# Kernel tuning notes

Hardware: AMD Instinct MI355X
Metric: run time of the kernel (lower is better)

Reference implementation:

```python
import jax, jax.numpy as jnp
import numpy as np

NUM_HEADS = 16


def setup_inputs() -> dict:
    key = jax.random.key(0)
    k1, k2, k3, k4 = jax.random.split(key, 4)
    in_dim, out_dim = 1024, 1024
    x = jax.random.normal(k1, (4, 2048, in_dim), dtype=jnp.float32)
    # nn.Linear weights stored as [out, in]; we keep that convention.
    s = 1.0 / np.sqrt(in_dim)
    Wq = jax.random.uniform(k2, (out_dim, in_dim), jnp.float32, -s, s)
    Wk = jax.random.uniform(k3, (out_dim, in_dim), jnp.float32, -s, s)
    Wv = jax.random.uniform(k4, (out_dim, in_dim), jnp.float32, -s, s)
    return {"x": x, "Wq": Wq, "Wk": Wk, "Wv": Wv}


def reference(x, Wq, Wk, Wv):
    b, n, _ = x.shape
    out_dim = Wq.shape[0]
    h = NUM_HEADS
    d = out_dim // h  # head_dim

    def split_heads(t):  # [b,n,out] -> [b,h,n,d]
        return t.reshape(b, n, h, d).transpose(0, 2, 1, 3)

    q = split_heads(x @ Wq.T)
    k = split_heads(x @ Wk.T)
    v = split_heads(x @ Wv.T)

    scores = jnp.einsum("bhqd,bhkd->bhqk", q, k) / jnp.sqrt(jnp.float32(d))
    causal = jnp.tril(jnp.ones((n, n), dtype=bool))
    scores = jnp.where(causal, scores, -jnp.inf)
    attn = jax.nn.softmax(scores, axis=-1)
    out = jnp.einsum("bhqk,bhkd->bhqd", attn, v)
    return out.transpose(0, 2, 1, 3).reshape(b, n, out_dim)
```

## Files before the change

### kernel.cpp

```cpp
#include <hip/hip_runtime.h>

typedef __attribute__((ext_vector_type(8))) short short8;
typedef __attribute__((ext_vector_type(4))) short short4v;
typedef __attribute__((ext_vector_type(4))) float floatx4;
typedef __attribute__((ext_vector_type(16))) float floatx16;

#define GLOBAL_AS __attribute__((address_space(1)))
#define LDS_AS __attribute__((address_space(3)))

__device__ __forceinline__ short f2bs(float f) {
    union { float f; unsigned u; } v; v.f = f;
    unsigned r = v.u + 0x7fffu + ((v.u >> 16) & 1u);
    return (short)(r >> 16);
}

#if __has_builtin(__builtin_amdgcn_cvt_pk_bf16_f32)
typedef __attribute__((ext_vector_type(2))) __bf16 bf16x2;
__device__ __forceinline__ unsigned pk2(float a, float b) {
    union { bf16x2 v; unsigned u; } u;
    u.v = __builtin_amdgcn_cvt_pk_bf16_f32(a, b);
    return u.u;
}
#else
__device__ __forceinline__ unsigned pk2(float a, float b) {
    union { float f; unsigned u; } x, y; x.f = a; y.f = b;
    return ((y.u + 0x8000u) & 0xffff0000u) | ((x.u + 0x8000u) >> 16);
}
#endif

__global__ __launch_bounds__(256) void cast_all(const float* __restrict__ x,
                                                const float* __restrict__ Wq,
                                                const float* __restrict__ Wk,
                                                const float* __restrict__ Wv,
                                                short* __restrict__ xb,
                                                short* __restrict__ wb) {
    int b = blockIdx.x;
    int t = threadIdx.x;
    const float* src;
    short* dst;
    int idx;
    if (b < 8192) {
        src = x; dst = xb; idx = b * 1024 + t * 4;
    } else {
        int r = b - 8192;
        int wz = r >> 10;
        src = (wz == 0) ? Wq : (wz == 1) ? Wk : Wv;
        dst = wb + wz * (1 << 20);
        idx = (r & 1023) * 1024 + t * 4;
    }
    float4 v = *(const float4*)(src + idx);
    short4v o;
    o.x = f2bs(v.x); o.y = f2bs(v.y); o.z = f2bs(v.z); o.w = f2bs(v.w);
    *(short4v*)(dst + idx) = o;
}

__global__ __launch_bounds__(256) void qkv_gemm(const short* __restrict__ xb,
                                                const short* __restrict__ wb,
                                                short* __restrict__ qout,
                                                short* __restrict__ kout,
                                                short* __restrict__ vtout) {
    __shared__ short As[128 * 64];
    __shared__ short Bs[128 * 64];
    const int K = 1024;
    int tid = threadIdx.x;
    int lane = tid & 63;
    int wid = tid >> 6;
    int quad = lane >> 4;
    int l16 = lane & 15;
    int wm = (wid >> 1) * 64;
    int wn = (wid & 1) * 64;
    int bm = blockIdx.x * 128;
    int bn = blockIdx.y * 128;
    const short* W = wb + (size_t)blockIdx.z * K * 1024;

    floatx4 acc[4][4];
#pragma unroll
    for (int i = 0; i < 4; i++)
#pragma unroll
        for (int j = 0; j < 4; j++) acc[i][j] = (floatx4){0.f, 0.f, 0.f, 0.f};

    int srow = tid >> 3;
    int ssw = ((tid & 7) ^ (srow & 7)) * 8;

    for (int kk = 0; kk < K; kk += 64) {
        __syncthreads();
#pragma unroll
        for (int l = 0; l < 4; l++) {
            const short* g = xb + (size_t)(bm + srow + l * 32) * K + kk + ssw;
            __builtin_amdgcn_global_load_lds((const GLOBAL_AS void*)g,
                                             (LDS_AS void*)(As + tid * 8 + l * 2048), 16, 0, 0);
        }
#pragma unroll
        for (int l = 0; l < 4; l++) {
            const short* g = W + (size_t)(bn + srow + l * 32) * K + kk + ssw;
            __builtin_amdgcn_global_load_lds((const GLOBAL_AS void*)g,
                                             (LDS_AS void*)(Bs + tid * 8 + l * 2048), 16, 0, 0);
        }
        __syncthreads();

#pragma unroll
        for (int s = 0; s < 2; s++) {
            int slot = ((s * 4 + quad) ^ (l16 & 7)) * 8;
            short8 af[4], bf[4];
#pragma unroll
            for (int i = 0; i < 4; i++)
                af[i] = *(const short8*)(As + (wm + i * 16 + l16) * 64 + slot);
#pragma unroll
            for (int j = 0; j < 4; j++)
                bf[j] = *(const short8*)(Bs + (wn + j * 16 + l16) * 64 + slot);
#pragma unroll
            for (int i = 0; i < 4; i++)
#pragma unroll
                for (int j = 0; j < 4; j++)
                    acc[i][j] = __builtin_amdgcn_mfma_f32_16x16x32_bf16(af[i], bf[j], acc[i][j], 0, 0, 0);
        }
    }

    if (blockIdx.z == 2) {
#pragma unroll
        for (int i = 0; i < 4; i++) {
#pragma unroll
            for (int j = 0; j < 4; j++) {
                int m = bm + wm + i * 16 + quad * 4;
                int c = bn + wn + j * 16 + l16;
                int b = m >> 11, nn = m & 2047, h = c >> 6, dd = c & 63;
                short4v pk;
                pk.x = f2bs(acc[i][j][0]);
                pk.y = f2bs(acc[i][j][1]);
                pk.z = f2bs(acc[i][j][2]);
                pk.w = f2bs(acc[i][j][3]);
                *(short4v*)(vtout + ((size_t)(b * 16 + h) * 64 + dd) * 2048 + nn) = pk;
            }
        }
    } else {
        short* dst = (blockIdx.z == 0) ? qout : kout;
        float qs = (blockIdx.z == 0) ? 0.180336881f : 1.0f;
#pragma unroll
        for (int i = 0; i < 4; i++) {
#pragma unroll
            for (int j = 0; j < 4; j++) {
#pragma unroll
                for (int r = 0; r < 4; r++) {
                    int m = bm + wm + i * 16 + quad * 4 + r;
                    int c = bn + wn + j * 16 + l16;
                    dst[((size_t)((m >> 11) * 16 + (c >> 6)) * 2048 + (m & 2047)) * 64 + (c & 63)] =
                        f2bs(acc[i][j][r] * qs);
                }
            }
        }
    }
}

__global__ __launch_bounds__(256, 2) void attn(const short* __restrict__ q,
                                               const short* __restrict__ k,
                                               const short* __restrict__ vt,
                                               float* __restrict__ out) {
    __shared__ short Ks[128 * 64];
    __shared__ short Vs[64 * 128];
    __shared__ short Ps[4 * 32 * 136];

    int tid = threadIdx.x;
    int lane = tid & 63;
    int wid = tid >> 6;
    int l32 = lane & 31;
    int half = lane >> 5;

    int flat = blockIdx.x;
    int xcd = flat & 7;
    int slot = flat >> 3;
    int bh = xcd * 8 + (slot >> 3);
    int qx = slot & 7;
    int b = bh >> 4, h = bh & 15;

    const short* qp = q + (size_t)(b * 16 + h) * 2048 * 64;
    const short* kp = k + (size_t)(b * 16 + h) * 2048 * 64;
    const short* vp = vt + (size_t)(b * 16 + h) * 64 * 2048;

    int krow = tid >> 3;
    int ksw = ((tid & 7) ^ (krow & 7)) * 8;
    int vd = tid >> 4;
    int vc = tid & 15;
    int vsw = ((vc & 8) | ((vc ^ vd) & 7)) * 8;

    short* pw = Ps + wid * (32 * 136);

    for (int phase = 0; phase < 2; phase++) {
        int qt = (phase == 0) ? qx : (15 - qx);
        int qbase = qt * 128;
        int qrow_w = qbase + wid * 32;
        int qlane = qrow_w + l32;

        short8 qf[4];
#pragma unroll
        for (int s = 0; s < 4; s++)
            qf[s] = *(const short8*)(qp + (size_t)qlane * 64 + s * 16 + half * 8);

        floatx16 oacc[2];
#pragma unroll
        for (int nt = 0; nt < 2; nt++)
#pragma unroll
            for (int e = 0; e < 16; e++) oacc[nt][e] = 0.f;
        float rs = 0.f;

        int ntiles = qt + 1;
        for (int t = 0; t < ntiles; t++) {
            int kvb = t * 128;
            __syncthreads();
#pragma unroll
            for (int l = 0; l < 4; l++) {
                const short* g = kp + (size_t)(kvb + krow + l * 32) * 64 + ksw;
                __builtin_amdgcn_global_load_lds((const GLOBAL_AS void*)g,
                                                 (LDS_AS void*)(Ks + tid * 8 + l * 2048), 16, 0, 0);
            }
#pragma unroll
            for (int l = 0; l < 4; l++) {
                const short* g = vp + (size_t)(vd + l * 16) * 2048 + kvb + vsw;
                __builtin_amdgcn_global_load_lds((const GLOBAL_AS void*)g,
                                                 (LDS_AS void*)(Vs + tid * 8 + l * 2048), 16, 0, 0);
            }
            __syncthreads();

            floatx16 sacc[4];
#pragma unroll
            for (int kb = 0; kb < 4; kb++)
#pragma unroll
                for (int e = 0; e < 16; e++) sacc[kb][e] = 0.f;
#pragma unroll
            for (int s = 0; s < 4; s++) {
#pragma unroll
                for (int kb = 0; kb < 4; kb++) {
                    int key = kb * 32 + l32;
                    int c = s * 2 + half;
                    short8 kf = *(const short8*)(Ks + key * 64 + ((c ^ (key & 7)) * 8));
                    sacc[kb] = __builtin_amdgcn_mfma_f32_32x32x16_bf16(kf, qf[s], sacc[kb], 0, 0, 0);
                }
            }

            bool diag = (t == ntiles - 1) && (phase >= 0) && (kvb + 127 > qrow_w);
#pragma unroll
            for (int kb = 0; kb < 4; kb++) {
#pragma unroll
                for (int e = 0; e < 16; e++) {
                    float p = __builtin_amdgcn_exp2f(sacc[kb][e]);
                    if (diag) {
                        int key = kvb + kb * 32 + (e & 3) + 8 * (e >> 2) + 4 * half;
                        p = (key > qlane) ? 0.f : p;
                    }
                    sacc[kb][e] = p;
                    rs += p;
                }
#pragma unroll
                for (int g = 0; g < 4; g++) {
                    int2 wv;
                    wv.x = pk2(sacc[kb][4 * g], sacc[kb][4 * g + 1]);
                    wv.y = pk2(sacc[kb][4 * g + 2], sacc[kb][4 * g + 3]);
                    *(int2*)(pw + l32 * 136 + kb * 32 + g * 8 + 4 * half) = wv;
                }
            }
            __threadfence_block();

#pragma unroll
            for (int s = 0; s < 8; s++) {
                short8 pf = *(const short8*)(pw + l32 * 136 + s * 16 + half * 8);
#pragma unroll
                for (int nt = 0; nt < 2; nt++) {
                    int d = nt * 32 + l32;
                    int c = s * 2 + half;
                    int sl = (c & 8) | ((c ^ (d & 7)) & 7);
                    short8 vf = *(const short8*)(Vs + d * 128 + sl * 8);
                    oacc[nt] = __builtin_amdgcn_mfma_f32_32x32x16_bf16(pf, vf, oacc[nt], 0, 0, 0);
                }
            }
        }

        float tot = rs + __shfl_xor(rs, 32);
        float inv = 1.0f / tot;
        float invr[16];
#pragma unroll
        for (int e = 0; e < 16; e++)
            invr[e] = __shfl(inv, (e & 3) + 8 * (e >> 2) + 4 * half);
#pragma unroll
        for (int nt = 0; nt < 2; nt++) {
#pragma unroll
            for (int e = 0; e < 16; e++) {
                int r = (e & 3) + 8 * (e >> 2) + 4 * half;
                int nn = qrow_w + r;
                out[((size_t)b * 2048 + nn) * 1024 + h * 64 + nt * 32 + l32] = oacc[nt][e] * invr[e];
            }
        }
    }
}

extern "C" void kernel_launch(void* const* d_in, const int* in_sizes, int n_in,
                              void* d_out, int out_size, void* d_ws, size_t ws_size,
                              hipStream_t stream) {
    const float* x = (const float*)d_in[0];
    const float* Wq = (const float*)d_in[1];
    const float* Wk = (const float*)d_in[2];
    const float* Wv = (const float*)d_in[3];
    float* out = (float*)d_out;
    char* ws = (char*)d_ws;

    short* xb = (short*)ws;
    short* wb = (short*)(ws + (16u << 20));
    short* qb = (short*)(ws + (22u << 20));
    short* kb = (short*)(ws + (38u << 20));
    short* vtb = (short*)(ws + (54u << 20));

    cast_all<<<8192 + 3 * 1024, 256, 0, stream>>>(x, Wq, Wk, Wv, xb, wb);
    qkv_gemm<<<dim3(64, 8, 3), 256, 0, stream>>>(xb, wb, qb, kb, vtb);
    attn<<<512, 256, 0, stream>>>(qb, kb, vtb, out);
}
```

Measured before the change: 206.9 us.

## Rewrite QKV GEMM as 256x256 double-buffered pipelined tiles with grid swizzle

The QKV projection GEMM moves from 128x128 tiles with 256 threads and a load-then-compute loop to 256x256 tiles with 512 threads. Global-to-LDS loads for the next K-step are double-buffered and interleaved with the MFMA quadrants, using explicit barriers, waitcnts and setprio. A flattened, swizzled grid treats Q, K and V as one 3072-column GEMM. The aim is to overlap memory with compute and raise data reuse, at the cost of 128KB of LDS and high register pressure, with only 384 blocks to spread across the CUs.

```diff
diff --git a/kernel.cpp b/kernel.cpp
--- a/kernel.cpp
+++ b/kernel.cpp
@@ -54,97 +54,146 @@
     *(short4v*)(dst + idx) = o;
 }
 
-__global__ __launch_bounds__(256) void qkv_gemm(const short* __restrict__ xb,
-                                                const short* __restrict__ wb,
-                                                short* __restrict__ qout,
-                                                short* __restrict__ kout,
-                                                short* __restrict__ vtout) {
-    __shared__ short As[128 * 64];
-    __shared__ short Bs[128 * 64];
+__global__ __launch_bounds__(512, 2) void qkv_gemm(const short* __restrict__ xb,
+                                                   const short* __restrict__ wb,
+                                                   short* __restrict__ qout,
+                                                   short* __restrict__ kout,
+                                                   short* __restrict__ vtout) {
+    __shared__ short As[32768];
+    __shared__ short Bs[32768];
     const int K = 1024;
     int tid = threadIdx.x;
     int lane = tid & 63;
     int wid = tid >> 6;
     int quad = lane >> 4;
     int l16 = lane & 15;
-    int wm = (wid >> 1) * 64;
-    int wn = (wid & 1) * 64;
-    int bm = blockIdx.x * 128;
-    int bn = blockIdx.y * 128;
-    const short* W = wb + (size_t)blockIdx.z * K * 1024;
-
-    floatx4 acc[4][4];
-#pragma unroll
-    for (int i = 0; i < 4; i++)
+    int wm = (wid >> 2) * 128;
+    int wn = (wid & 3) * 64;
+
+    int flat = blockIdx.x;
+    int swz = (flat & 7) * 48 + (flat >> 3);
+    int bx = swz / 12;
+    int by = swz - bx * 12;
+    int bm = bx * 256;
+
+    const short* A0 = xb + (size_t)bm * K;
+    const short* B0 = wb + (size_t)(by * 256) * K;
+
+    int srow = tid >> 3;
+    int sw = ((tid & 7) ^ (srow & 7)) * 8;
+    const short* gA = A0 + (size_t)srow * K + sw;
+    const short* gB = B0 + (size_t)(((tid >> 8) << 6) + (srow & 31)) * K + sw;
+    short* ldsA = As + tid * 8;
+    short* ldsB = Bs + ((tid >> 8) << 12) + (tid & 255) * 8;
+
+#define STAGE_AU(nb, u, kkn) do { \
+    __builtin_amdgcn_global_load_lds((const GLOBAL_AS void*)(gA + (size_t)((u) * 64) * 1024 + (kkn)), \
+        (LDS_AS void*)(ldsA + (nb) * 16384 + (u) * 4096), 16, 0, 0); \
+    __builtin_amdgcn_global_load_lds((const GLOBAL_AS void*)(gA + (size_t)(128 + (u) * 64) * 1024 + (kkn)), \
+        (LDS_AS void*)(ldsA + (nb) * 16384 + 8192 + (u) * 4096), 16, 0, 0); \
+} while (0)
+#define STAGE_BU(nb, u, kkn) do { \
+    __builtin_amdgcn_global_load_lds((const GLOBAL_AS void*)(gB + (size_t)((u) * 32) * 1024 + (kkn)), \
+        (LDS_AS void*)(ldsB + (nb) * 16384 + (u) * 2048), 16, 0, 0); \
+    __builtin_amdgcn_global_load_lds((const GLOBAL_AS void*)(gB + (size_t)(128 + (u) * 32) * 1024 + (kkn)), \
+        (LDS_AS void*)(ldsB + (nb) * 16384 + 8192 + (u) * 2048), 16, 0, 0); \
+} while (0)
+
+#define BARX() __builtin_amdgcn_s_barrier()
+#define SBAR() __builtin_amdgcn_sched_barrier(0)
+#define LGKM0() asm volatile("s_waitcnt lgkmcnt(0)" ::: "memory")
+#define VM4() asm volatile("s_waitcnt vmcnt(4)" ::: "memory")
+
+#define LDA_(Ab, Qm) do { int xx = l16 & 7; \
+    _Pragma("unroll") for (int i = 0; i < 4; i++) { \
+        const short* rp = (Ab) + (wm + (Qm) * 64 + i * 16 + l16) * 64; \
+        aF[i][0] = *(const short8*)(rp + (quad ^ xx) * 8); \
+        aF[i][1] = *(const short8*)(rp + ((4 | quad) ^ xx) * 8); \
+    } } while (0)
+#define LDB_(Bb, Qn, bf) do { int xx = l16 & 7; \
+    _Pragma("unroll") for (int j = 0; j < 2; j++) { \
+        const short* rp = (Bb) + (wn + (Qn) * 32 + j * 16 + l16) * 64; \
+        bf[j][0] = *(const short8*)(rp + (quad ^ xx) * 8); \
+        bf[j][1] = *(const short8*)(rp + ((4 | quad) ^ xx) * 8); \
+    } } while (0)
+#define MM_(Qm, Qn, bf) do { \
+    __builtin_amdgcn_s_setprio(1); \
+    _Pragma("unroll") for (int s = 0; s < 2; s++) \
+    _Pragma("unroll") for (int i = 0; i < 4; i++) \
+    _Pragma("unroll") for (int j = 0; j < 2; j++) \
+        acc[(Qm) * 4 + i][(Qn) * 2 + j] = __builtin_amdgcn_mfma_f32_16x16x32_bf16( \
+            aF[i][s], bf[j][s], acc[(Qm) * 4 + i][(Qn) * 2 + j], 0, 0, 0); \
+    __builtin_amdgcn_s_setprio(0); \
+} while (0)
+
+    floatx4 acc[8][4];
+#pragma unroll
+    for (int i = 0; i < 8; i++)
 #pragma unroll
         for (int j = 0; j < 4; j++) acc[i][j] = (floatx4){0.f, 0.f, 0.f, 0.f};
-
-    int srow = tid >> 3;
-    int ssw = ((tid & 7) ^ (srow & 7)) * 8;
-
-    for (int kk = 0; kk < K; kk += 64) {
-        __syncthreads();
-#pragma unroll
-        for (int l = 0; l < 4; l++) {
-            const short* g = xb + (size_t)(bm + srow + l * 32) * K + kk + ssw;
-            __builtin_amdgcn_global_load_lds((const GLOBAL_AS void*)g,
-                                             (LDS_AS void*)(As + tid * 8 + l * 2048), 16, 0, 0);
-        }
-#pragma unroll
-        for (int l = 0; l < 4; l++) {
-            const short* g = W + (size_t)(bn + srow + l * 32) * K + kk + ssw;
-            __builtin_amdgcn_global_load_lds((const GLOBAL_AS void*)g,
-                                             (LDS_AS void*)(Bs + tid * 8 + l * 2048), 16, 0, 0);
-        }
-        __syncthreads();
-
-#pragma unroll
-        for (int s = 0; s < 2; s++) {
-            int slot = ((s * 4 + quad) ^ (l16 & 7)) * 8;
-            short8 af[4], bf[4];
-#pragma unroll
-            for (int i = 0; i < 4; i++)
-                af[i] = *(const short8*)(As + (wm + i * 16 + l16) * 64 + slot);
-#pragma unroll
-            for (int j = 0; j < 4; j++)
-                bf[j] = *(const short8*)(Bs + (wn + j * 16 + l16) * 64 + slot);
-#pragma unroll
-            for (int i = 0; i < 4; i++)
-#pragma unroll
-                for (int j = 0; j < 4; j++)
-                    acc[i][j] = __builtin_amdgcn_mfma_f32_16x16x32_bf16(af[i], bf[j], acc[i][j], 0, 0, 0);
-        }
+    short8 aF[4][2], bF0[2][2], bF1[2][2];
+
+    STAGE_AU(0, 0, 0); STAGE_BU(0, 0, 0); STAGE_BU(0, 1, 0); STAGE_AU(0, 1, 0);
+    VM4(); BARX(); SBAR();
+
+#pragma unroll 2
+    for (int T = 0; T < 16; T++) {
+        const short* Ab = As + (T & 1) * 16384;
+        const short* Bb = Bs + (T & 1) * 16384;
+        int nb = (T & 1) ^ 1;
+        int kkn = ((T + 1) & 15) << 6;
+        LDA_(Ab, 0); LDB_(Bb, 0, bF0);
+        STAGE_AU(nb, 0, kkn);
+        BARX(); LGKM0(); SBAR();
+        MM_(0, 0, bF0);
+        VM4(); BARX(); SBAR();
+        LDB_(Bb, 1, bF1);
+        STAGE_BU(nb, 0, kkn);
+        BARX(); LGKM0(); SBAR();
+        MM_(0, 1, bF1);
+        VM4(); BARX(); SBAR();
+        LDA_(Ab, 1);
+        STAGE_BU(nb, 1, kkn);
+        BARX(); LGKM0(); SBAR();
+        MM_(1, 1, bF1);
+        BARX(); SBAR();
+        STAGE_AU(nb, 1, kkn);
+        BARX(); SBAR();
+        MM_(1, 0, bF0);
+        VM4(); BARX(); SBAR();
     }
 
-    if (blockIdx.z == 2) {
-#pragma unroll
-        for (int i = 0; i < 4; i++) {
-#pragma unroll
-            for (int j = 0; j < 4; j++) {
-                int m = bm + wm + i * 16 + quad * 4;
-                int c = bn + wn + j * 16 + l16;
+    int wz = by >> 2;
+    int cb = (by & 3) * 256 + wn;
+    if (wz == 2) {
+#pragma unroll
+        for (int mi = 0; mi < 8; mi++) {
+#pragma unroll
+            for (int ni = 0; ni < 4; ni++) {
+                int m = bm + wm + mi * 16 + quad * 4;
+                int c = cb + ni * 16 + l16;
                 int b = m >> 11, nn = m & 2047, h = c >> 6, dd = c & 63;
                 short4v pk;
-                pk.x = f2bs(acc[i][j][0]);
-                pk.y = f2bs(acc[i][j][1]);
-                pk.z = f2bs(acc[i][j][2]);
-                pk.w = f2bs(acc[i][j][3]);
+                pk.x = f2bs(acc[mi][ni][0]);
+                pk.y = f2bs(acc[mi][ni][1]);
+                pk.z = f2bs(acc[mi][ni][2]);
+                pk.w = f2bs(acc[mi][ni][3]);
                 *(short4v*)(vtout + ((size_t)(b * 16 + h) * 64 + dd) * 2048 + nn) = pk;
             }
         }
     } else {
-        short* dst = (blockIdx.z == 0) ? qout : kout;
-        float qs = (blockIdx.z == 0) ? 0.180336881f : 1.0f;
-#pragma unroll
-        for (int i = 0; i < 4; i++) {
-#pragma unroll
-            for (int j = 0; j < 4; j++) {
+        short* dst = wz ? kout : qout;
+        float qs = wz ? 1.0f : 0.180336881f;
+#pragma unroll
+        for (int mi = 0; mi < 8; mi++) {
+#pragma unroll
+            for (int ni = 0; ni < 4; ni++) {
 #pragma unroll
                 for (int r = 0; r < 4; r++) {
-                    int m = bm + wm + i * 16 + quad * 4 + r;
-                    int c = bn + wn + j * 16 + l16;
+                    int m = bm + wm + mi * 16 + quad * 4 + r;
+                    int c = cb + ni * 16 + l16;
                     dst[((size_t)((m >> 11) * 16 + (c >> 6)) * 2048 + (m & 2047)) * 64 + (c & 63)] =
-                        f2bs(acc[i][j][r] * qs);
+                        f2bs(acc[mi][ni][r] * qs);
                 }
             }
         }
@@ -308,6 +357,6 @@
     short* vtb = (short*)(ws + (54u << 20));
 
     cast_all<<<8192 + 3 * 1024, 256, 0, stream>>>(x, Wq, Wk, Wv, xb, wb);
-    qkv_gemm<<<dim3(64, 8, 3), 256, 0, stream>>>(xb, wb, qb, kb, vtb);
+    qkv_gemm<<<384, 512, 0, stream>>>(xb, wb, qb, kb, vtb);
     attn<<<512, 256, 0, stream>>>(qb, kb, vtb, out);
 }
```

Result: no change. 207.7 us (+0.4%).

## Double-buffer K/V tiles and pass P via permlane32 swap instead of LDS

Applied to the files above, without the earlier changes.

Splits K and V into two LDS buffers and prefetches the next KV tile with global_load_lds while the current one is computed, using explicit vmcnt waits and s_barrier. The P matrix is no longer round-tripped through a per-wave LDS scratch. Its packed bf16 values are rearranged across half-waves with permlane32_swap into the MFMA A-operand layout. This hides load latency behind compute and removes LDS traffic for P, at the cost of twice the K/V LDS footprint, which could lower occupancy. It also depends on hand-tuned waitcnt counts being correct.

```diff
diff --git a/kernel.cpp b/kernel.cpp
--- a/kernel.cpp
+++ b/kernel.cpp
@@ -4,6 +4,7 @@
 typedef __attribute__((ext_vector_type(4))) short short4v;
 typedef __attribute__((ext_vector_type(4))) float floatx4;
 typedef __attribute__((ext_vector_type(16))) float floatx16;
+typedef __attribute__((ext_vector_type(2))) int iv2;
 
 #define GLOBAL_AS __attribute__((address_space(1)))
 #define LDS_AS __attribute__((address_space(3)))
@@ -155,9 +156,8 @@
                                                const short* __restrict__ k,
                                                const short* __restrict__ vt,
                                                float* __restrict__ out) {
-    __shared__ short Ks[128 * 64];
-    __shared__ short Vs[64 * 128];
-    __shared__ short Ps[4 * 32 * 136];
+    __shared__ short Ks[2][128 * 64];
+    __shared__ short Vs[2][64 * 128];
 
     int tid = threadIdx.x;
     int lane = tid & 63;
@@ -182,7 +182,18 @@
     int vc = tid & 15;
     int vsw = ((vc & 8) | ((vc ^ vd) & 7)) * 8;
 
-    short* pw = Ps + wid * (32 * 136);
+#define STAGE_KV(cb, kvb) do { \
+    _Pragma("unroll") for (int l = 0; l < 4; l++) { \
+        const short* g = kp + (size_t)((kvb) + krow + l * 32) * 64 + ksw; \
+        __builtin_amdgcn_global_load_lds((const GLOBAL_AS void*)g, \
+            (LDS_AS void*)(&Ks[cb][0] + tid * 8 + l * 2048), 16, 0, 0); \
+    } \
+    _Pragma("unroll") for (int l = 0; l < 4; l++) { \
+        const short* g = vp + (size_t)(vd + l * 16) * 2048 + (kvb) + vsw; \
+        __builtin_amdgcn_global_load_lds((const GLOBAL_AS void*)g, \
+            (LDS_AS void*)(&Vs[cb][0] + tid * 8 + l * 2048), 16, 0, 0); \
+    } \
+} while (0)
 
     for (int phase = 0; phase < 2; phase++) {
         int qt = (phase == 0) ? qx : (15 - qx);
@@ -203,22 +214,31 @@
         float rs = 0.f;
 
         int ntiles = qt + 1;
+
+        __builtin_amdgcn_sched_barrier(0);
+        __builtin_amdgcn_s_barrier();
+        __builtin_amdgcn_sched_barrier(0);
+        STAGE_KV(0, 0);
+
         for (int t = 0; t < ntiles; t++) {
+            int cur = t & 1;
             int kvb = t * 128;
-            __syncthreads();
-#pragma unroll
-            for (int l = 0; l < 4; l++) {
-                const short* g = kp + (size_t)(kvb + krow + l * 32) * 64 + ksw;
-                __builtin_amdgcn_global_load_lds((const GLOBAL_AS void*)g,
-                                                 (LDS_AS void*)(Ks + tid * 8 + l * 2048), 16, 0, 0);
-            }
-#pragma unroll
-            for (int l = 0; l < 4; l++) {
-                const short* g = vp + (size_t)(vd + l * 16) * 2048 + kvb + vsw;
-                __builtin_amdgcn_global_load_lds((const GLOBAL_AS void*)g,
-                                                 (LDS_AS void*)(Vs + tid * 8 + l * 2048), 16, 0, 0);
-            }
-            __syncthreads();
+
+            __builtin_amdgcn_sched_barrier(0);
+            __builtin_amdgcn_s_barrier();
+            __builtin_amdgcn_sched_barrier(0);
+            if (t + 1 < ntiles) {
+                STAGE_KV(cur ^ 1, kvb + 128);
+                asm volatile("s_waitcnt vmcnt(8)" ::: "memory");
+            } else {
+                asm volatile("s_waitcnt vmcnt(0)" ::: "memory");
+            }
+            __builtin_amdgcn_sched_barrier(0);
+            __builtin_amdgcn_s_barrier();
+            __builtin_amdgcn_sched_barrier(0);
+
+            const short* Kc = &Ks[cur][0];
+            const short* Vc = &Vs[cur][0];
 
             floatx16 sacc[4];
 #pragma unroll
@@ -231,12 +251,13 @@
                 for (int kb = 0; kb < 4; kb++) {
                     int key = kb * 32 + l32;
                     int c = s * 2 + half;
-                    short8 kf = *(const short8*)(Ks + key * 64 + ((c ^ (key & 7)) * 8));
+                    short8 kf = *(const short8*)(Kc + key * 64 + ((c ^ (key & 7)) * 8));
                     sacc[kb] = __builtin_amdgcn_mfma_f32_32x32x16_bf16(kf, qf[s], sacc[kb], 0, 0, 0);
                 }
             }
 
-            bool diag = (t == ntiles - 1) && (phase >= 0) && (kvb + 127 > qrow_w);
+            bool diag = (t == ntiles - 1) && (kvb + 127 > qrow_w);
+            unsigned W0[4][4], W1[4][4];
 #pragma unroll
             for (int kb = 0; kb < 4; kb++) {
 #pragma unroll
@@ -251,23 +272,27 @@
                 }
 #pragma unroll
                 for (int g = 0; g < 4; g++) {
-                    int2 wv;
-                    wv.x = pk2(sacc[kb][4 * g], sacc[kb][4 * g + 1]);
-                    wv.y = pk2(sacc[kb][4 * g + 2], sacc[kb][4 * g + 3]);
-                    *(int2*)(pw + l32 * 136 + kb * 32 + g * 8 + 4 * half) = wv;
-                }
-            }
-            __threadfence_block();
+                    W0[kb][g] = pk2(sacc[kb][4 * g + 0], sacc[kb][4 * g + 1]);
+                    W1[kb][g] = pk2(sacc[kb][4 * g + 2], sacc[kb][4 * g + 3]);
+                }
+            }
 
 #pragma unroll
             for (int s = 0; s < 8; s++) {
-                short8 pf = *(const short8*)(pw + l32 * 136 + s * 16 + half * 8);
+                int kb = s >> 1;
+                int g0 = (s & 1) * 2;
+                int g1 = g0 + 1;
+                iv2 r0 = __builtin_amdgcn_permlane32_swap(W0[kb][g0], W0[kb][g1], false, false);
+                iv2 r1 = __builtin_amdgcn_permlane32_swap(W1[kb][g0], W1[kb][g1], false, false);
+                union { int4 v; short8 s8; } pu;
+                pu.v.x = r0.x; pu.v.y = r1.x; pu.v.z = r0.y; pu.v.w = r1.y;
+                short8 pf = pu.s8;
 #pragma unroll
                 for (int nt = 0; nt < 2; nt++) {
                     int d = nt * 32 + l32;
                     int c = s * 2 + half;
                     int sl = (c & 8) | ((c ^ (d & 7)) & 7);
-                    short8 vf = *(const short8*)(Vs + d * 128 + sl * 8);
+                    short8 vf = *(const short8*)(Vc + d * 128 + sl * 8);
                     oacc[nt] = __builtin_amdgcn_mfma_f32_32x32x16_bf16(pf, vf, oacc[nt], 0, 0, 0);
                 }
             }
@@ -289,6 +314,7 @@
             }
         }
     }
+#undef STAGE_KV
 }
 
 extern "C" void kernel_launch(void* const* d_in, const int* in_sizes, int n_in,
```

Result: no change. 204.9 us (-1.0%).
